# Kernel optimization log

Hardware: AMD Instinct MI355X
Metric: run time of the kernel (lower is better)

## Reference

```python
import jax
import jax.numpy as jnp
from jax import lax
import numpy as np

B, C, H, W = 8, 1, 256, 256


def _edt(feat):
    """Exact Euclidean distance transform: distance from every pixel to the
    nearest True pixel in `feat` (bool [H, W]). Matches scipy's
    distance_transform_edt(~feature_background) semantics.

    Two-pass separable algorithm:
      1) exact 1D distance along axis 0 (two sequential scans),
      2) exact min-plus combine along axis 1:
         D^2(i,j) = min_l ( (j-l)^2 + g(i,l)^2 ).
    """
    h, w = feat.shape
    BIG = jnp.float32(h + w)  # larger than any achievable distance

    def step(c, row):
        d = jnp.where(row, jnp.float32(0.0), c + 1.0)
        return d, d

    _, d_fwd = lax.scan(step, jnp.full((w,), BIG, jnp.float32), feat)
    _, d_bwd = lax.scan(step, jnp.full((w,), BIG, jnp.float32), feat[::-1])
    g = jnp.minimum(d_fwd, d_bwd[::-1])  # [H, W] 1D distance along rows (axis 0)
    g2 = g * g

    j = jnp.arange(w, dtype=jnp.float32)
    off = (j[:, None] - j[None, :]) ** 2           # [W, W] (j - l)^2
    # d2[i, j] = min_l g2[i, l] + off[j, l]  -> [H, W, W] intermediate
    d2 = jnp.min(g2[:, None, :] + off[None, :, :], axis=2)
    return jnp.sqrt(d2)


def _sdf(mask):
    """Signed distance field for one bool mask [H, W]; zeros if mask is empty."""
    dist_out = _edt(mask)     # distance to nearest foreground pixel
    dist_in = _edt(~mask)     # distance to nearest background pixel
    sdf = dist_out - dist_in
    return jnp.where(mask.any(), sdf, jnp.zeros_like(sdf))


def setup_inputs() -> dict:
    key = jax.random.key(0)
    k1, k2 = jax.random.split(key)
    logits = jax.random.normal(k1, (B, C, H, W), dtype=jnp.float32)
    targets = jax.random.randint(k2, (B, C, H, W), 0, 2, dtype=jnp.int32)
    return {"logits": logits, "targets": targets}


def reference(logits, targets):
    probs = jax.nn.sigmoid(logits)          # [B, 1, H, W]
    mask = targets[:, 0] != 0               # bool [B, H, W]
    sdf = jax.vmap(_sdf)(mask)              # [B, H, W]
    per_sample = jnp.mean(probs[:, 0] * sdf, axis=(1, 2))  # [B]
    return jnp.mean(per_sample)
```

## Files before the change

### kernel.cpp

```cpp
#include <hip/hip_runtime.h>
#include <math.h>

#define BB 8
#define HH 256
#define WW 256
#define PAD 16
#define LDSW (WW + 2 * PAD + 4)
#define NROW (BB * HH)


__global__ void build_colbits_kernel(const int* __restrict__ targets,
                                     unsigned int* __restrict__ colbits,
                                     int* __restrict__ blockany) {
    const int b = blockIdx.x;
    const int w = blockIdx.y;
    const int j = threadIdx.x;
    const int* t = targets + ((size_t)b * HH + 32 * w) * WW + j;
    unsigned int bits = 0u;
    #pragma unroll
    for (int r = 0; r < 32; ++r)
        bits |= (unsigned int)(t[r * WW] != 0) << r;
    colbits[((size_t)(b * WW + j) << 3) + w] = bits;

    __shared__ int anyw[4];
    const unsigned long long ba = __ballot(bits != 0u);
    if ((j & 63) == 0) anyw[j >> 6] = (ba != 0ull) ? 1 : 0;
    __syncthreads();
    if (j == 0)
        blockany[b * 8 + w] = anyw[0] | anyw[1] | anyw[2] | anyw[3];
}

__device__ __forceinline__ float col_dist(unsigned long long w0, unsigned long long w1,
                                          unsigned long long w2, unsigned long long w3,
                                          int i) {
    const int INF = 1 << 20;
    int best = min(i + 513, 768 - i);
    const unsigned long long ws[4] = {w0, w1, w2, w3};
    #pragma unroll
    for (int k = 0; k < 4; ++k) {
        const unsigned long long wk = ws[k];
        const int rel = i - 64 * k;
        {
            const int sh = min(max(rel, 0), 63);
            const unsigned long long m = (rel < 64) ? (wk >> sh) : 0ull;
            const int d = m ? (__ffsll((unsigned long long)m) - 1 + sh - rel) : INF;
            best = min(best, d);
        }
        {
            const int sh = min(max(63 - rel, 0), 63);
            const unsigned long long m = (rel >= 0) ? (wk << sh) : 0ull;
            const int add = rel > 63 ? rel - 63 : 0;
            const int d = m ? (__clzll((long long)m) + add) : INF;
            best = min(best, d);
        }
    }
    return (float)best;
}

__global__ void fused_row_kernel(const float* __restrict__ logits,
                                 const unsigned long long* __restrict__ colbits,
                                 double* __restrict__ partial) {
    const int row = blockIdx.x;
    const int b = row >> 8;
    const int i = row & 255;
    const int j = threadIdx.x;
    const int lane = j & 63;
    const int wid  = j >> 6;

    __shared__ __align__(16) float sbuf[2][LDSW];
    __shared__ float hred[4];
    __shared__ double wsum[4];

    const unsigned long long* cb = colbits + ((size_t)(b * WW + j) << 2);
    const unsigned long long w0 = cb[0], w1 = cb[1], w2 = cb[2], w3 = cb[3];
    const float x = logits[(size_t)row * WW + j];

    const unsigned long long wsel = (i < 64) ? w0 : (i < 128) ? w1 : (i < 192) ? w2 : w3;
    const bool m = ((wsel >> (i & 63)) & 1ull) != 0ull;

    const float go = col_dist(w0, w1, w2, w3, i);
    const float gi = col_dist(~w0, ~w1, ~w2, ~w3, i);
    const float go2 = go * go, gi2 = gi * gi;
    sbuf[0][PAD + j] = go2;
    sbuf[1][PAD + j] = gi2;
    if (j < PAD) {
        sbuf[0][j] = 1e30f;            sbuf[1][j] = 1e30f;
        sbuf[0][PAD + WW + j] = 1e30f; sbuf[1][PAD + WW + j] = 1e30f;
    }

    float hmax = m ? gi2 : go2;
    #pragma unroll
    for (int off = 32; off > 0; off >>= 1)
        hmax = fmaxf(hmax, __shfl_xor(hmax, off, 64));
    if (lane == 0) hred[wid] = hmax;
    __syncthreads();
    hmax = fmaxf(fmaxf(hred[0], hred[1]), fmaxf(hred[2], hred[3]));

    const float* s = &sbuf[m ? 1 : 0][PAD];
    float d2 = 1e30f;
    if (hmax <= 288.0f) {
        const float* sw = s + j - PAD;
        float df = (float)PAD;
        #pragma unroll
        for (int k = 0; k <= 2 * PAD; ++k) {
            d2 = fminf(d2, fmaf(df, df, sw[k]));
            df -= 1.0f;
        }
    } else {
        float df = (float)j;
        #pragma unroll 8
        for (int l = 0; l < WW; ++l) {
            d2 = fminf(d2, fmaf(df, df, s[l]));
            df -= 1.0f;
        }
    }

    const double sd = sqrt((double)d2);
    const double sdf = m ? -sd : sd;
    const double p  = 1.0 / (1.0 + exp(-(double)x));
    double c = p * sdf;

    #pragma unroll
    for (int off = 32; off > 0; off >>= 1)
        c += __shfl_down(c, off, 64);
    if (lane == 0) wsum[wid] = c;
    __syncthreads();
    if (j == 0)
        partial[row] = wsum[0] + wsum[1] + wsum[2] + wsum[3];
}

__global__ void finalize_kernel(const double* __restrict__ partial,
                                const int* __restrict__ blockany,
                                float* __restrict__ out) {
    const int t = threadIdx.x;
    double s = 0.0;
    #pragma unroll
    for (int b = 0; b < BB; ++b) {
        int f = 0;
        #pragma unroll
        for (int w = 0; w < 8; ++w) f |= blockany[b * 8 + w];
        const double v = partial[b * HH + t];
        s += f ? v : 0.0;
    }
    #pragma unroll
    for (int off = 32; off > 0; off >>= 1)
        s += __shfl_down(s, off, 64);
    __shared__ double wsum[4];
    if ((t & 63) == 0) wsum[t >> 6] = s;
    __syncthreads();
    if (t == 0)
        out[0] = (float)((wsum[0] + wsum[1] + wsum[2] + wsum[3])
                         / (double)((long long)BB * HH * WW));
}

extern "C" void kernel_launch(void* const* d_in, const int* in_sizes, int n_in,
                              void* d_out, int out_size, void* d_ws, size_t ws_size,
                              hipStream_t stream) {
    const float* logits  = (const float*)d_in[0];
    const int*   targets = (const int*)d_in[1];
    float*       out     = (float*)d_out;

    char* ws = (char*)d_ws;
    const size_t off_bits = 0;
    const size_t off_any  = (size_t)BB * WW * 8 * sizeof(unsigned int);
    const size_t off_par  = off_any + 256;

    unsigned int* colbits  = (unsigned int*)(ws + off_bits);
    int*          blockany = (int*)(ws + off_any);
    double*       partial  = (double*)(ws + off_par);

    build_colbits_kernel<<<dim3(BB, 8), WW, 0, stream>>>(targets, colbits, blockany);
    fused_row_kernel<<<NROW, WW, 0, stream>>>(logits,
                                              (const unsigned long long*)colbits,
                                              partial);
    finalize_kernel<<<1, WW, 0, stream>>>(partial, blockany, out);
}
```

Before: 18.45 us.

## Compute one column distance per pixel, add narrower window, spread bit-pack over more blocks

```diff
diff --git a/kernel.cpp b/kernel.cpp
--- a/kernel.cpp
+++ b/kernel.cpp
@@ -10,24 +10,24 @@
 
 
 __global__ void build_colbits_kernel(const int* __restrict__ targets,
-                                     unsigned int* __restrict__ colbits,
+                                     unsigned char* __restrict__ colbits,
                                      int* __restrict__ blockany) {
     const int b = blockIdx.x;
     const int w = blockIdx.y;
     const int j = threadIdx.x;
-    const int* t = targets + ((size_t)b * HH + 32 * w) * WW + j;
+    const int* t = targets + ((size_t)b * HH + 8 * w) * WW + j;
     unsigned int bits = 0u;
     #pragma unroll
-    for (int r = 0; r < 32; ++r)
+    for (int r = 0; r < 8; ++r)
         bits |= (unsigned int)(t[r * WW] != 0) << r;
-    colbits[((size_t)(b * WW + j) << 3) + w] = bits;
+    colbits[((size_t)(b * WW + j) << 5) + w] = (unsigned char)bits;
 
     __shared__ int anyw[4];
     const unsigned long long ba = __ballot(bits != 0u);
     if ((j & 63) == 0) anyw[j >> 6] = (ba != 0ull) ? 1 : 0;
     __syncthreads();
     if (j == 0)
-        blockany[b * 8 + w] = anyw[0] | anyw[1] | anyw[2] | anyw[3];
+        blockany[b * 32 + w] = anyw[0] | anyw[1] | anyw[2] | anyw[3];
 }
 
 __device__ __forceinline__ float col_dist(unsigned long long w0, unsigned long long w1,
@@ -58,7 +58,7 @@
 }
 
 __global__ void fused_row_kernel(const float* __restrict__ logits,
-                                 const unsigned long long* __restrict__ colbits,
+                                 const unsigned char* __restrict__ colbits,
                                  double* __restrict__ partial) {
     const int row = blockIdx.x;
     const int b = row >> 8;
@@ -71,24 +71,27 @@
     __shared__ float hred[4];
     __shared__ double wsum[4];
 
-    const unsigned long long* cb = colbits + ((size_t)(b * WW + j) << 2);
-    const unsigned long long w0 = cb[0], w1 = cb[1], w2 = cb[2], w3 = cb[3];
+    const ulonglong2* cb =
+        (const ulonglong2*)(colbits + ((size_t)(b * WW + j) << 5));
+    const ulonglong2 lo = cb[0], hi = cb[1];
+    const unsigned long long w0 = lo.x, w1 = lo.y, w2 = hi.x, w3 = hi.y;
     const float x = logits[(size_t)row * WW + j];
 
     const unsigned long long wsel = (i < 64) ? w0 : (i < 128) ? w1 : (i < 192) ? w2 : w3;
     const bool m = ((wsel >> (i & 63)) & 1ull) != 0ull;
 
-    const float go = col_dist(w0, w1, w2, w3, i);
-    const float gi = col_dist(~w0, ~w1, ~w2, ~w3, i);
-    const float go2 = go * go, gi2 = gi * gi;
-    sbuf[0][PAD + j] = go2;
-    sbuf[1][PAD + j] = gi2;
+    const unsigned long long inv = m ? ~0ull : 0ull;
+    const float d = col_dist(w0 ^ inv, w1 ^ inv, w2 ^ inv, w3 ^ inv, i);
+    const float d2v = d * d;
+
+    sbuf[0][PAD + j] = m ? 0.0f : d2v;
+    sbuf[1][PAD + j] = m ? d2v : 0.0f;
     if (j < PAD) {
         sbuf[0][j] = 1e30f;            sbuf[1][j] = 1e30f;
         sbuf[0][PAD + WW + j] = 1e30f; sbuf[1][PAD + WW + j] = 1e30f;
     }
 
-    float hmax = m ? gi2 : go2;
+    float hmax = d2v;
     #pragma unroll
     for (int off = 32; off > 0; off >>= 1)
         hmax = fmaxf(hmax, __shfl_xor(hmax, off, 64));
@@ -98,7 +101,15 @@
 
     const float* s = &sbuf[m ? 1 : 0][PAD];
     float d2 = 1e30f;
-    if (hmax <= 288.0f) {
+    if (hmax <= 100.0f) {
+        const float* sw = s + j - 10;
+        float df = 10.0f;
+        #pragma unroll
+        for (int k = 0; k <= 20; ++k) {
+            d2 = fminf(d2, fmaf(df, df, sw[k]));
+            df -= 1.0f;
+        }
+    } else if (hmax <= 288.0f) {
         const float* sw = s + j - PAD;
         float df = (float)PAD;
         #pragma unroll
@@ -138,7 +149,7 @@
     for (int b = 0; b < BB; ++b) {
         int f = 0;
         #pragma unroll
-        for (int w = 0; w < 8; ++w) f |= blockany[b * 8 + w];
+        for (int w = 0; w < 32; ++w) f |= blockany[b * 32 + w];
         const double v = partial[b * HH + t];
         s += f ? v : 0.0;
     }
@@ -162,16 +173,14 @@
 
     char* ws = (char*)d_ws;
     const size_t off_bits = 0;
-    const size_t off_any  = (size_t)BB * WW * 8 * sizeof(unsigned int);
-    const size_t off_par  = off_any + 256;
+    const size_t off_any  = (size_t)BB * WW * 32;
+    const size_t off_par  = off_any + (size_t)BB * 32 * sizeof(int);
 
-    unsigned int* colbits  = (unsigned int*)(ws + off_bits);
-    int*          blockany = (int*)(ws + off_any);
-    double*       partial  = (double*)(ws + off_par);
+    unsigned char* colbits  = (unsigned char*)(ws + off_bits);
+    int*           blockany = (int*)(ws + off_any);
+    double*        partial  = (double*)(ws + off_par);
 
-    build_colbits_kernel<<<dim3(BB, 8), WW, 0, stream>>>(targets, colbits, blockany);
-    fused_row_kernel<<<NROW, WW, 0, stream>>>(logits,
-                                              (const unsigned long long*)colbits,
-                                              partial);
+    build_colbits_kernel<<<dim3(BB, 32), WW, 0, stream>>>(targets, colbits, blockany);
+    fused_row_kernel<<<NROW, WW, 0, stream>>>(logits, colbits, partial);
     finalize_kernel<<<1, WW, 0, stream>>>(partial, blockany, out);
 }
```

Result: slower. 20.16 us (+9.3%).
